# Performance work log

Measured on AMD Instinct MI355X. Metric: run time of the kernel, lower is better.

## Reference

```python
import jax, jax.numpy as jnp
import numpy as np

# Dims: B walkers, NELEC electrons split equally into NSPIN=2 spins of NE each,
# D backflow feature dim, NION ions, SPATIAL=3 spatial dims, NORB orbitals/spin.
B, NELEC, D, NION, SPATIAL, NORB = 1024, 64, 32, 16, 3, 32
NSPIN = 2
NE = NELEC // NSPIN


def setup_inputs() -> dict:
    key = jax.random.key(0)
    ks = jax.random.split(key, 6)
    x = jax.random.normal(ks[0], (B, NELEC, D), jnp.float32)
    r_ei = jax.random.normal(ks[1], (B, NELEC, NION, SPATIAL), jnp.float32)
    # per-spin Dense(norbitals) on concatenated pair features [y_p, y_i] (2D -> NORB)
    W_orb = jax.random.normal(ks[2], (NSPIN, 2 * D, NORB), jnp.float32) / np.sqrt(2 * D)
    b_orb = jax.random.normal(ks[3], (NSPIN, NORB), jnp.float32) * 0.01
    # anisotropic decay: a 3x3 matrix per (spin, ion, orbital)
    W_env_dim = jax.random.normal(ks[4], (NSPIN, NION, SPATIAL, NORB, SPATIAL), jnp.float32) / np.sqrt(SPATIAL)
    # linear combination over ions (Dense(1), no bias)
    w_env_ion = jax.random.normal(ks[5], (NSPIN, NION), jnp.float32) / np.sqrt(NION)
    return dict(x=x, r_ei=r_ei, W_orb=W_orb, b_orb=b_orb,
                W_env_dim=W_env_dim, w_env_ion=w_env_ion)


def reference(x, r_ei, W_orb, b_orb, W_env_dim, w_env_ion):
    # Equal spin split -> stack spins as a leading axis (s = NSPIN)
    xs = jnp.stack(jnp.split(x, NSPIN, axis=-2), axis=0)       # (s, B, NE, D)
    res = jnp.stack(jnp.split(r_ei, NSPIN, axis=-3), axis=0)   # (s, B, NE, NION, 3)

    # Pairwise doubly-equivariant inputs: pair[p, i] = concat(y_p, y_i)
    xp = jnp.broadcast_to(xs[:, :, :, None, :], (NSPIN, B, NE, NE, D))
    xi = jnp.broadcast_to(xs[:, :, None, :, :], (NSPIN, B, NE, NE, D))
    pair = jnp.concatenate([xp, xi], axis=-1)                  # (s, B, NE, NE, 2D)
    orbs = jnp.einsum('sbpif,sfo->sbpio', pair, W_orb) + b_orb[:, None, None, None, :]

    # Anisotropic exponential envelope: exp(-||A_{ion,orb} (r - R_ion)||), combined over ions
    scale = jnp.einsum('sbnid,sidoe->sbnoie', res, W_env_dim)  # (s, B, NE, NORB, NION, 3)
    dist = jnp.linalg.norm(scale, axis=-1)                     # (s, B, NE, NORB, NION)
    env = jnp.einsum('sbnoi,si->sbno', jnp.exp(-dist), w_env_ion)  # (s, B, NE, NORB)

    # envelope depends on electron i (axis -2 of orbs), broadcast over p (axis -3)
    return orbs * env[:, :, None, :, :]                        # (s, B, NE, NE, NORB)
```

## Files before the change

### kernel.cpp

```cpp
#include <hip/hip_runtime.h>

#define BATCH 1024
#define NELEC 64
#define DF    32
#define NION  16
#define NORB  32
#define NE    32
#define NSB   2048
#define FACT_FLOATS (NSB * NE * NORB)
#define WS_NEEDED   ((size_t)3 * FACT_FLOATS * 4)

__global__ __launch_bounds__(256) void k1_factors(
    const float* __restrict__ x,
    const float* __restrict__ r_ei,
    const float* __restrict__ W_orb,
    const float* __restrict__ b_orb,
    const float* __restrict__ W_env,
    const float* __restrict__ w_ion,
    float* __restrict__ Uf,
    float* __restrict__ Ef,
    float* __restrict__ Wf)
{
    __shared__ float sx[NE][DF];
    __shared__ float sworb[2*DF][NORB];
    __shared__ float sr[NE][NION*3];
    __shared__ float swe[NION*3*NORB*3];
    __shared__ float sb[NORB];
    __shared__ float swion[NION];

    const int t   = threadIdx.x;
    const int blk = blockIdx.x;
    const int s   = blk >> 10;
    const int b   = blk & (BATCH - 1);

    {
        const float4* xg = (const float4*)(x + (size_t)(b*NELEC + s*NE) * DF);
        ((float4*)&sx[0][0])[t] = xg[t];
    }
    {
        const float4* wg = (const float4*)(W_orb + (size_t)s * 2*DF*NORB);
        float4* d = (float4*)&sworb[0][0];
        d[t]       = wg[t];
        d[t + 256] = wg[t + 256];
    }
    {
        const float4* rg = (const float4*)(r_ei + (size_t)(b*NELEC + s*NE) * NION * 3);
        float4* d = (float4*)&sr[0][0];
        d[t] = rg[t];
        if (t < 128) d[t + 256] = rg[t + 256];
    }
    {
        const float4* weg = (const float4*)(W_env + (size_t)s * NION*3*NORB*3);
        float4* d = (float4*)swe;
        for (int j = t; j < 1152; j += 256) d[j] = weg[j];
    }
    if (t < NORB) sb[t]    = b_orb[s*NORB + t];
    if (t < NION) swion[t] = w_ion[s*NION + t];
    __syncthreads();

    const int o  = t & 31;
    const int ng = t >> 5;

    float u_acc[4], v_acc[4];
    #pragma unroll
    for (int uu = 0; uu < 4; ++uu) { u_acc[uu] = 0.f; v_acc[uu] = 0.f; }
    #pragma unroll
    for (int d = 0; d < DF; ++d) {
        const float w0 = sworb[d][o];
        const float w1 = sworb[DF + d][o];
        #pragma unroll
        for (int uu = 0; uu < 4; ++uu) {
            const float xv = sx[ng*4 + uu][d];
            u_acc[uu] += xv * w0;
            v_acc[uu] += xv * w1;
        }
    }

    float e_acc[4] = {0.f, 0.f, 0.f, 0.f};
    #pragma unroll
    for (int i = 0; i < NION; ++i) {
        const float* wp = &swe[i*3*NORB*3 + o*3];
        const float w00 = wp[0],          w01 = wp[1],          w02 = wp[2];
        const float w10 = wp[NORB*3],     w11 = wp[NORB*3+1],   w12 = wp[NORB*3+2];
        const float w20 = wp[2*NORB*3],   w21 = wp[2*NORB*3+1], w22 = wp[2*NORB*3+2];
        const float wi  = swion[i];
        #pragma unroll
        for (int uu = 0; uu < 4; ++uu) {
            const int n = ng*4 + uu;
            const float r0 = sr[n][i*3 + 0];
            const float r1 = sr[n][i*3 + 1];
            const float r2 = sr[n][i*3 + 2];
            const float s0 = r0*w00 + r1*w10 + r2*w20;
            const float s1 = r0*w01 + r1*w11 + r2*w21;
            const float s2 = r0*w02 + r1*w12 + r2*w22;
            const float dist = sqrtf(s0*s0 + s1*s1 + s2*s2);
            e_acc[uu] += __expf(-dist) * wi;
        }
    }

    const size_t base = (size_t)blk * (NE*NORB);
    #pragma unroll
    for (int uu = 0; uu < 4; ++uu) {
        const int n = ng*4 + uu;
        Uf[base + n*NORB + o] = u_acc[uu];
        Ef[base + n*NORB + o] = e_acc[uu];
        Wf[base + n*NORB + o] = (v_acc[uu] + sb[o]) * e_acc[uu];
    }
}

__global__ __launch_bounds__(256) void k2_expand(
    const float* __restrict__ Uf,
    const float* __restrict__ Ef,
    const float* __restrict__ Wf,
    float* __restrict__ out)
{
    __shared__ float sU[NE][NORB];
    const int t   = threadIdx.x;
    const int blk = blockIdx.x;
    const size_t base = (size_t)blk * (NE*NORB);

    ((float4*)&sU[0][0])[t] = ((const float4*)(Uf + base))[t];
    const float4 e4 = ((const float4*)(Ef + base))[t];
    const float4 w4 = ((const float4*)(Wf + base))[t];
    __syncthreads();

    const int o0 = (t & 7) * 4;
    float4* outp = (float4*)(out + (size_t)blk * (NE*NE*NORB));
    #pragma unroll
    for (int p = 0; p < NE; ++p) {
        const float4 u4 = *(const float4*)&sU[p][o0];
        float4 r;
        r.x = u4.x*e4.x + w4.x;
        r.y = u4.y*e4.y + w4.y;
        r.z = u4.z*e4.z + w4.z;
        r.w = u4.w*e4.w + w4.w;
        outp[p*256 + t] = r;
    }
}

__global__ __launch_bounds__(256) void deq_orbital_fused(
    const float* __restrict__ x, const float* __restrict__ r_ei,
    const float* __restrict__ W_orb, const float* __restrict__ b_orb,
    const float* __restrict__ W_env, const float* __restrict__ w_ion,
    float* __restrict__ out)
{
    __shared__ float sx[NE][DF];
    __shared__ float sworb[2*DF][NORB];
    __shared__ float sr[NE][NION*3];
    __shared__ float swe[NION*3*NORB*3];
    __shared__ float sU[NE][NORB];
    __shared__ float sV[NE][NORB];
    __shared__ float sE[NE][NORB];
    __shared__ float sb[NORB];
    __shared__ float swion[NION];

    const int t   = threadIdx.x;
    const int blk = blockIdx.x;
    const int s   = blk >> 10;
    const int b   = blk & (BATCH - 1);

    {
        const float4* xg = (const float4*)(x + (size_t)(b*NELEC + s*NE) * DF);
        ((float4*)&sx[0][0])[t] = xg[t];
    }
    {
        const float4* wg = (const float4*)(W_orb + (size_t)s * 2*DF*NORB);
        float4* d = (float4*)&sworb[0][0];
        d[t] = wg[t]; d[t + 256] = wg[t + 256];
    }
    {
        const float4* rg = (const float4*)(r_ei + (size_t)(b*NELEC + s*NE) * NION * 3);
        float4* d = (float4*)&sr[0][0];
        d[t] = rg[t];
        if (t < 128) d[t + 256] = rg[t + 256];
    }
    {
        const float4* weg = (const float4*)(W_env + (size_t)s * NION*3*NORB*3);
        float4* d = (float4*)swe;
        for (int j = t; j < 1152; j += 256) d[j] = weg[j];
    }
    if (t < NORB) sb[t]    = b_orb[s*NORB + t];
    if (t < NION) swion[t] = w_ion[s*NION + t];
    __syncthreads();

    const int o  = t & 31;
    const int ng = t >> 5;
    float u_acc[4], v_acc[4];
    #pragma unroll
    for (int uu = 0; uu < 4; ++uu) { u_acc[uu] = 0.f; v_acc[uu] = 0.f; }
    #pragma unroll
    for (int d = 0; d < DF; ++d) {
        const float w0 = sworb[d][o];
        const float w1 = sworb[DF + d][o];
        #pragma unroll
        for (int uu = 0; uu < 4; ++uu) {
            const float xv = sx[ng*4 + uu][d];
            u_acc[uu] += xv * w0;
            v_acc[uu] += xv * w1;
        }
    }
    #pragma unroll
    for (int uu = 0; uu < 4; ++uu) {
        sU[ng*4 + uu][o] = u_acc[uu];
        sV[ng*4 + uu][o] = v_acc[uu];
    }
    #pragma unroll
    for (int uu = 0; uu < 4; ++uu) {
        const int n = ng*4 + uu;
        float acc = 0.f;
        #pragma unroll
        for (int i = 0; i < NION; ++i) {
            const float r0 = sr[n][i*3 + 0];
            const float r1 = sr[n][i*3 + 1];
            const float r2 = sr[n][i*3 + 2];
            const float* wp = &swe[i*3*NORB*3 + o*3];
            const float s0 = r0*wp[0] + r1*wp[NORB*3    ] + r2*wp[2*NORB*3    ];
            const float s1 = r0*wp[1] + r1*wp[NORB*3 + 1] + r2*wp[2*NORB*3 + 1];
            const float s2 = r0*wp[2] + r1*wp[NORB*3 + 2] + r2*wp[2*NORB*3 + 2];
            const float dist = sqrtf(s0*s0 + s1*s1 + s2*s2);
            acc += __expf(-dist) * swion[i];
        }
        sE[n][o] = acc;
        sV[n][o] = (v_acc[uu] + sb[o]) * acc;
    }
    __syncthreads();

    const int io = t >> 3;
    const int o0 = (t & 7) * 4;
    const float4 e4 = *(const float4*)&sE[io][o0];
    const float4 w4 = *(const float4*)&sV[io][o0];
    float4* outp = (float4*)(out + (size_t)blk * (NE*NE*NORB));
    #pragma unroll
    for (int p = 0; p < NE; ++p) {
        const float4 u4 = *(const float4*)&sU[p][o0];
        float4 r;
        r.x = u4.x*e4.x + w4.x;
        r.y = u4.y*e4.y + w4.y;
        r.z = u4.z*e4.z + w4.z;
        r.w = u4.w*e4.w + w4.w;
        outp[p*256 + t] = r;
    }
}

extern "C" void kernel_launch(void* const* d_in, const int* in_sizes, int n_in,
                              void* d_out, int out_size, void* d_ws, size_t ws_size,
                              hipStream_t stream) {
    const float* x     = (const float*)d_in[0];
    const float* r_ei  = (const float*)d_in[1];
    const float* W_orb = (const float*)d_in[2];
    const float* b_orb = (const float*)d_in[3];
    const float* W_env = (const float*)d_in[4];
    const float* w_ion = (const float*)d_in[5];
    float* out = (float*)d_out;

    if (ws_size >= WS_NEEDED) {
        float* Uf = (float*)d_ws;
        float* Ef = Uf + FACT_FLOATS;
        float* Wf = Ef + FACT_FLOATS;
        k1_factors<<<NSB, 256, 0, stream>>>(x, r_ei, W_orb, b_orb, W_env, w_ion,
                                            Uf, Ef, Wf);
        k2_expand<<<NSB, 256, 0, stream>>>(Uf, Ef, Wf, out);
    } else {
        deq_orbital_fused<<<NSB, 256, 0, stream>>>(x, r_ei, W_orb, b_orb,
                                                   W_env, w_ion, out);
    }
}
```

Before: 84.63 us.

## Precompute envelope Gram matrices and process two walkers per factor block

A new tiny kernel precomputes, for each (spin, ion, orbital), the 6 unique entries of the symmetric Gram matrix A^T A of the envelope matrix. The factor kernel then gets the squared distance as a quadratic form in r (6 FMAs instead of 9 plus 3), with a clamp at zero. The factor kernel also now handles two walkers per block with float4 register tiling over orbitals, and reads x directly from global memory. It adds one extra launch and can lose a little precision from the quadratic-form evaluation.

After: 125.4 us. 1.48x slower.

```diff
diff --git a/kernel.cpp b/kernel.cpp
--- a/kernel.cpp
+++ b/kernel.cpp
@@ -8,104 +8,162 @@
 #define NE    32
 #define NSB   2048
 #define FACT_FLOATS (NSB * NE * NORB)
-#define WS_NEEDED   ((size_t)3 * FACT_FLOATS * 4)
-
-__global__ __launch_bounds__(256) void k1_factors(
+#define M_PAD 8192
+#define WS_NEEDED ((size_t)(M_PAD + 3 * FACT_FLOATS) * 4)
+
+#define FMA4(acc, sc, v) { acc.x += (sc)*(v).x; acc.y += (sc)*(v).y; acc.z += (sc)*(v).z; acc.w += (sc)*(v).w; }
+
+__global__ __launch_bounds__(256) void k0_gram(
+    const float* __restrict__ W_env,
+    float* __restrict__ Mg)
+{
+    int id = blockIdx.x * 256 + threadIdx.x;
+    if (id >= 2 * NION * NORB) return;
+    int s = id >> 9, rem = id & 511, i = rem >> 5, o = rem & 31;
+    const float* base = W_env + ((size_t)((s*NION + i) * 3) * NORB + o) * 3;
+    float a0[3], a1[3], a2[3];
+    #pragma unroll
+    for (int e = 0; e < 3; ++e) {
+        a0[e] = base[e];
+        a1[e] = base[96 + e];
+        a2[e] = base[192 + e];
+    }
+    float* out = Mg + ((size_t)(s*NION + i) * NORB + o) * 6;
+    out[0] = a0[0]*a0[0] + a0[1]*a0[1] + a0[2]*a0[2];
+    out[1] = a1[0]*a1[0] + a1[1]*a1[1] + a1[2]*a1[2];
+    out[2] = a2[0]*a2[0] + a2[1]*a2[1] + a2[2]*a2[2];
+    out[3] = 2.f*(a0[0]*a1[0] + a0[1]*a1[1] + a0[2]*a1[2]);
+    out[4] = 2.f*(a0[0]*a2[0] + a0[1]*a2[1] + a0[2]*a2[2]);
+    out[5] = 2.f*(a1[0]*a2[0] + a1[1]*a2[1] + a1[2]*a2[2]);
+}
+
+__global__ __launch_bounds__(256, 4) void k1_factors2(
     const float* __restrict__ x,
     const float* __restrict__ r_ei,
     const float* __restrict__ W_orb,
     const float* __restrict__ b_orb,
-    const float* __restrict__ W_env,
     const float* __restrict__ w_ion,
-    float* __restrict__ Uf,
-    float* __restrict__ Ef,
-    float* __restrict__ Wf)
+    const float* __restrict__ Mg,
+    float* __restrict__ Uf, float* __restrict__ Ef, float* __restrict__ Wf)
 {
-    __shared__ float sx[NE][DF];
-    __shared__ float sworb[2*DF][NORB];
-    __shared__ float sr[NE][NION*3];
-    __shared__ float swe[NION*3*NORB*3];
-    __shared__ float sb[NORB];
+    __shared__ float sworb[2*DF*NORB];
+    __shared__ float sM[NION*NORB*6];
+    __shared__ float sr[64*52];
     __shared__ float swion[NION];
 
     const int t   = threadIdx.x;
     const int blk = blockIdx.x;
-    const int s   = blk >> 10;
-    const int b   = blk & (BATCH - 1);
-
-    {
-        const float4* xg = (const float4*)(x + (size_t)(b*NELEC + s*NE) * DF);
-        ((float4*)&sx[0][0])[t] = xg[t];
-    }
-    {
-        const float4* wg = (const float4*)(W_orb + (size_t)s * 2*DF*NORB);
-        float4* d = (float4*)&sworb[0][0];
-        d[t]       = wg[t];
-        d[t + 256] = wg[t + 256];
-    }
-    {
-        const float4* rg = (const float4*)(r_ei + (size_t)(b*NELEC + s*NE) * NION * 3);
-        float4* d = (float4*)&sr[0][0];
-        d[t] = rg[t];
-        if (t < 128) d[t + 256] = rg[t + 256];
-    }
-    {
-        const float4* weg = (const float4*)(W_env + (size_t)s * NION*3*NORB*3);
-        float4* d = (float4*)swe;
-        for (int j = t; j < 1152; j += 256) d[j] = weg[j];
-    }
-    if (t < NORB) sb[t]    = b_orb[s*NORB + t];
+    const int s   = blk >> 9;
+    const int b0  = (blk & 511) * 2;
+
+    {
+        const float4* g = (const float4*)(W_orb + (size_t)s * 2*DF*NORB);
+        float4* d = (float4*)sworb;
+        d[t] = g[t]; d[t + 256] = g[t + 256];
+    }
+    {
+        const float4* g = (const float4*)(Mg + (size_t)s * NION*NORB*6);
+        float4* d = (float4*)sM;
+        d[t] = g[t]; d[t + 256] = g[t + 256]; d[t + 512] = g[t + 512];
+    }
+    {
+        const int row = t >> 2, seg = t & 3;
+        const int w = row >> 5, nn = row & 31;
+        const float4* g = (const float4*)(r_ei + ((size_t)(b0 + w)*NELEC + s*NE + nn) * NION * 3);
+        float4 v0 = g[seg*3 + 0], v1 = g[seg*3 + 1], v2 = g[seg*3 + 2];
+        float4* d = (float4*)(sr + row*52 + seg*12);
+        d[0] = v0; d[1] = v1; d[2] = v2;
+    }
     if (t < NION) swion[t] = w_ion[s*NION + t];
     __syncthreads();
 
-    const int o  = t & 31;
-    const int ng = t >> 5;
-
-    float u_acc[4], v_acc[4];
-    #pragma unroll
-    for (int uu = 0; uu < 4; ++uu) { u_acc[uu] = 0.f; v_acc[uu] = 0.f; }
-    #pragma unroll
-    for (int d = 0; d < DF; ++d) {
-        const float w0 = sworb[d][o];
-        const float w1 = sworb[DF + d][o];
+    const int n  = t >> 3;
+    const int o0 = (t & 7) * 4;
+
+    float4 uA = {0,0,0,0}, uB = {0,0,0,0}, vA = {0,0,0,0}, vB = {0,0,0,0};
+    const float* xrowA = x + ((size_t)(b0 + 0)*NELEC + s*NE + n) * DF;
+    const float* xrowB = x + ((size_t)(b0 + 1)*NELEC + s*NE + n) * DF;
+    #pragma unroll
+    for (int db = 0; db < 8; ++db) {
+        const float4 xa = *(const float4*)(xrowA + db*4);
+        const float4 xb = *(const float4*)(xrowB + db*4);
         #pragma unroll
-        for (int uu = 0; uu < 4; ++uu) {
-            const float xv = sx[ng*4 + uu][d];
-            u_acc[uu] += xv * w0;
-            v_acc[uu] += xv * w1;
+        for (int k = 0; k < 4; ++k) {
+            const int d = db*4 + k;
+            const float4 w0 = *(const float4*)(sworb + d*NORB + o0);
+            const float4 w1 = *(const float4*)(sworb + (DF + d)*NORB + o0);
+            const float xk0 = (&xa.x)[k], xk1 = (&xb.x)[k];
+            FMA4(uA, xk0, w0); FMA4(vA, xk0, w1);
+            FMA4(uB, xk1, w0); FMA4(vB, xk1, w1);
         }
     }
 
-    float e_acc[4] = {0.f, 0.f, 0.f, 0.f};
-    #pragma unroll
-    for (int i = 0; i < NION; ++i) {
-        const float* wp = &swe[i*3*NORB*3 + o*3];
-        const float w00 = wp[0],          w01 = wp[1],          w02 = wp[2];
-        const float w10 = wp[NORB*3],     w11 = wp[NORB*3+1],   w12 = wp[NORB*3+2];
-        const float w20 = wp[2*NORB*3],   w21 = wp[2*NORB*3+1], w22 = wp[2*NORB*3+2];
-        const float wi  = swion[i];
+    float4 eA = {0,0,0,0}, eB = {0,0,0,0};
+    const float* rpA = sr + n*52;
+    const float* rpB = sr + (32 + n)*52;
+    #pragma unroll
+    for (int ig = 0; ig < 4; ++ig) {
+        float rA[12], rB[12];
+        *(float4*)(rA + 0) = *(const float4*)(rpA + ig*12 + 0);
+        *(float4*)(rA + 4) = *(const float4*)(rpA + ig*12 + 4);
+        *(float4*)(rA + 8) = *(const float4*)(rpA + ig*12 + 8);
+        *(float4*)(rB + 0) = *(const float4*)(rpB + ig*12 + 0);
+        *(float4*)(rB + 4) = *(const float4*)(rpB + ig*12 + 4);
+        *(float4*)(rB + 8) = *(const float4*)(rpB + ig*12 + 8);
         #pragma unroll
-        for (int uu = 0; uu < 4; ++uu) {
-            const int n = ng*4 + uu;
-            const float r0 = sr[n][i*3 + 0];
-            const float r1 = sr[n][i*3 + 1];
-            const float r2 = sr[n][i*3 + 2];
-            const float s0 = r0*w00 + r1*w10 + r2*w20;
-            const float s1 = r0*w01 + r1*w11 + r2*w21;
-            const float s2 = r0*w02 + r1*w12 + r2*w22;
-            const float dist = sqrtf(s0*s0 + s1*s1 + s2*s2);
-            e_acc[uu] += __expf(-dist) * wi;
+        for (int ii = 0; ii < 4; ++ii) {
+            const int i = ig*4 + ii;
+            const float* mp = sM + (size_t)(i*NORB + o0) * 6;
+            float mA[24];
+            *(float4*)(mA +  0) = *(const float4*)(mp +  0);
+            *(float4*)(mA +  4) = *(const float4*)(mp +  4);
+            *(float4*)(mA +  8) = *(const float4*)(mp +  8);
+            *(float4*)(mA + 12) = *(const float4*)(mp + 12);
+            *(float4*)(mA + 16) = *(const float4*)(mp + 16);
+            *(float4*)(mA + 20) = *(const float4*)(mp + 20);
+            const float wi = swion[i];
+            {
+                const float r0 = rA[ii*3+0], r1 = rA[ii*3+1], r2 = rA[ii*3+2];
+                const float q00 = r0*r0, q11 = r1*r1, q22 = r2*r2;
+                const float q01 = r0*r1, q02 = r0*r2, q12 = r1*r2;
+                #pragma unroll
+                for (int j = 0; j < 4; ++j) {
+                    const float* m = mA + j*6;
+                    float d2 = m[0]*q00 + m[1]*q11 + m[2]*q22
+                             + m[3]*q01 + m[4]*q02 + m[5]*q12;
+                    d2 = fmaxf(d2, 0.f);
+                    (&eA.x)[j] += wi * __expf(-sqrtf(d2));
+                }
+            }
+            {
+                const float r0 = rB[ii*3+0], r1 = rB[ii*3+1], r2 = rB[ii*3+2];
+                const float q00 = r0*r0, q11 = r1*r1, q22 = r2*r2;
+                const float q01 = r0*r1, q02 = r0*r2, q12 = r1*r2;
+                #pragma unroll
+                for (int j = 0; j < 4; ++j) {
+                    const float* m = mA + j*6;
+                    float d2 = m[0]*q00 + m[1]*q11 + m[2]*q22
+                             + m[3]*q01 + m[4]*q02 + m[5]*q12;
+                    d2 = fmaxf(d2, 0.f);
+                    (&eB.x)[j] += wi * __expf(-sqrtf(d2));
+                }
+            }
         }
     }
 
-    const size_t base = (size_t)blk * (NE*NORB);
-    #pragma unroll
-    for (int uu = 0; uu < 4; ++uu) {
-        const int n = ng*4 + uu;
-        Uf[base + n*NORB + o] = u_acc[uu];
-        Ef[base + n*NORB + o] = e_acc[uu];
-        Wf[base + n*NORB + o] = (v_acc[uu] + sb[o]) * e_acc[uu];
-    }
+    const float4 bq = *(const float4*)(b_orb + s*NORB + o0);
+    const size_t wbase = ((size_t)(s*BATCH + b0)) * (NE*NORB) + (size_t)t * 4;
+    float4 wA, wB;
+    wA.x = (vA.x + bq.x) * eA.x; wA.y = (vA.y + bq.y) * eA.y;
+    wA.z = (vA.z + bq.z) * eA.z; wA.w = (vA.w + bq.w) * eA.w;
+    wB.x = (vB.x + bq.x) * eB.x; wB.y = (vB.y + bq.y) * eB.y;
+    wB.z = (vB.z + bq.z) * eB.z; wB.w = (vB.w + bq.w) * eB.w;
+    *(float4*)(Uf + wbase)             = uA;
+    *(float4*)(Ef + wbase)             = eA;
+    *(float4*)(Wf + wbase)             = wA;
+    *(float4*)(Uf + wbase + NE*NORB)   = uB;
+    *(float4*)(Ef + wbase + NE*NORB)   = eB;
+    *(float4*)(Wf + wbase + NE*NORB)   = wB;
 }
 
 __global__ __launch_bounds__(256) void k2_expand(
@@ -206,13 +264,13 @@
     }
     #pragma unroll
     for (int uu = 0; uu < 4; ++uu) {
-        const int n = ng*4 + uu;
+        const int nn = ng*4 + uu;
         float acc = 0.f;
         #pragma unroll
         for (int i = 0; i < NION; ++i) {
-            const float r0 = sr[n][i*3 + 0];
-            const float r1 = sr[n][i*3 + 1];
-            const float r2 = sr[n][i*3 + 2];
+            const float r0 = sr[nn][i*3 + 0];
+            const float r1 = sr[nn][i*3 + 1];
+            const float r2 = sr[nn][i*3 + 2];
             const float* wp = &swe[i*3*NORB*3 + o*3];
             const float s0 = r0*wp[0] + r1*wp[NORB*3    ] + r2*wp[2*NORB*3    ];
             const float s1 = r0*wp[1] + r1*wp[NORB*3 + 1] + r2*wp[2*NORB*3 + 1];
@@ -220,8 +278,8 @@
             const float dist = sqrtf(s0*s0 + s1*s1 + s2*s2);
             acc += __expf(-dist) * swion[i];
         }
-        sE[n][o] = acc;
-        sV[n][o] = (v_acc[uu] + sb[o]) * acc;
+        sE[nn][o] = acc;
+        sV[nn][o] = (v_acc[uu] + sb[o]) * acc;
     }
     __syncthreads();
 
@@ -254,11 +312,13 @@
     float* out = (float*)d_out;
 
     if (ws_size >= WS_NEEDED) {
-        float* Uf = (float*)d_ws;
+        float* Mg = (float*)d_ws;
+        float* Uf = Mg + M_PAD;
         float* Ef = Uf + FACT_FLOATS;
         float* Wf = Ef + FACT_FLOATS;
-        k1_factors<<<NSB, 256, 0, stream>>>(x, r_ei, W_orb, b_orb, W_env, w_ion,
-                                            Uf, Ef, Wf);
+        k0_gram<<<4, 256, 0, stream>>>(W_env, Mg);
+        k1_factors2<<<1024, 256, 0, stream>>>(x, r_ei, W_orb, b_orb, w_ion, Mg,
+                                              Uf, Ef, Wf);
         k2_expand<<<NSB, 256, 0, stream>>>(Uf, Ef, Wf, out);
     } else {
         deq_orbital_fused<<<NSB, 256, 0, stream>>>(x, r_ei, W_orb, b_orb,
```
